# Kernel tuning notes

Hardware: AMD Instinct MI355X
Metric: run time of the kernel (lower is better)

Reference implementation:

```python
import jax, jax.numpy as jnp
import numpy as np

C = 256
HEADS = 4
RADIUS = 2
LN_EPS = 1e-5


def setup_inputs() -> dict:
    key = jax.random.key(0)
    ks = jax.random.split(key, 8)
    s = 0.02
    return {
        "feat": jax.random.normal(ks[0], (8, C, 64, 64), dtype=jnp.float32),
        "in_w": jax.random.normal(ks[1], (3 * C, C), dtype=jnp.float32) * s,
        "in_b": jnp.zeros((3 * C,), dtype=jnp.float32),
        "out_w": jax.random.normal(ks[2], (C, C), dtype=jnp.float32) * s,
        "out_b": jnp.zeros((C,), dtype=jnp.float32),
        "proj_w": jax.random.normal(ks[3], (C, 4 * C), dtype=jnp.float32) * s,
        "proj_b": jnp.zeros((C,), dtype=jnp.float32),
        "ln_g": jnp.ones((C,), dtype=jnp.float32),
        "ln_b": jnp.zeros((C,), dtype=jnp.float32),
    }


def _spatial_mask(h, w, radius):
    yy, xx = jnp.meshgrid(jnp.arange(h), jnp.arange(w), indexing="ij")
    coords = jnp.stack([yy.ravel(), xx.ravel()], axis=-1).astype(jnp.float32)  # [N,2]
    dist = jnp.abs(coords[:, None, :] - coords[None, :, :]).sum(-1)  # Manhattan [N,N]
    return jnp.where(dist > radius, -jnp.inf, 0.0).astype(jnp.float32)


def _attend(qf, mf, mask, in_w, in_b, out_w, out_b, proj_w, proj_b, ln_g, ln_b):
    b, c, h, w = qf.shape
    n = h * w
    d = c // HEADS
    qt = qf.reshape(b, c, n).transpose(0, 2, 1)  # [B,N,C]
    mt = mf.reshape(b, c, n).transpose(0, 2, 1)
    q = qt @ in_w[:c].T + in_b[:c]
    k = mt @ in_w[c:2 * c].T + in_b[c:2 * c]
    v = mt @ in_w[2 * c:].T + in_b[2 * c:]
    # [B,H,N,D]
    q = q.reshape(b, n, HEADS, d).transpose(0, 2, 1, 3)
    k = k.reshape(b, n, HEADS, d).transpose(0, 2, 1, 3)
    v = v.reshape(b, n, HEADS, d).transpose(0, 2, 1, 3)
    scores = jnp.einsum("bhnd,bhmd->bhnm", q, k) / jnp.sqrt(jnp.float32(d)) + mask
    attn = jax.nn.softmax(scores, axis=-1)
    ctx = jnp.einsum("bhnm,bhmd->bhnd", attn, v)
    ctx = ctx.transpose(0, 2, 1, 3).reshape(b, n, c) @ out_w.T + out_b  # [B,N,C]
    asym = jnp.concatenate([qt, ctx, jnp.abs(qt - ctx), qt * ctx], axis=-1)
    y = asym @ proj_w.T + proj_b
    mu = y.mean(-1, keepdims=True)
    var = ((y - mu) ** 2).mean(-1, keepdims=True)
    y = (y - mu) / jnp.sqrt(var + LN_EPS) * ln_g + ln_b
    y = jax.nn.relu(y)
    return y.transpose(0, 2, 1).reshape(b, c, h, w)


def reference(feat, in_w, in_b, out_w, out_b, proj_w, proj_b, ln_g, ln_b):
    b, c, h, w = feat.shape
    mid = w // 2
    left = feat[:, :, :, :mid]
    right = feat[:, :, :, mid:]
    right_mirror = right[:, :, :, ::-1]
    left_mirror = left[:, :, :, ::-1]
    mask = _spatial_mask(h, mid, RADIUS)
    args = (mask, in_w, in_b, out_w, out_b, proj_w, proj_b, ln_g, ln_b)
    left_asym = _attend(left, right_mirror, *args)
    right_asym = _attend(right, left_mirror, *args)
    return jnp.concatenate([left_asym, right_asym], axis=-1)
```

## Files before the change

kernel.cpp:

```cpp
#include <hip/hip_runtime.h>
#include <hip/hip_bf16.h>


#define NTOK 32768

using bf16x8 = __attribute__((ext_vector_type(8))) short;
using f32x4  = __attribute__((ext_vector_type(4))) float;

__device__ __forceinline__ float b2f(short s) {
    unsigned u = ((unsigned)(unsigned short)s) << 16;
    union { unsigned u; float f; } c; c.u = u; return c.f;
}
__device__ __forceinline__ short f2b(float f) {
    __hip_bfloat16 h = __float2bfloat16(f);
    return *(short*)&h;
}
__device__ __forceinline__ void async_copy16(const void* g, void* l) {
    __builtin_amdgcn_global_load_lds(
        (const __attribute__((address_space(1))) unsigned int*)g,
        (__attribute__((address_space(3))) unsigned int*)l, 16, 0, 0);
}

__global__ __launch_bounds__(256) void prep_kernel(const float* __restrict__ feat,
                                                   const float* __restrict__ in_w,
                                                   const float* __restrict__ out_w,
                                                   const float* __restrict__ proj_w,
                                                   __hip_bfloat16* __restrict__ X,
                                                   __hip_bfloat16* __restrict__ wbf) {
    const int bid = blockIdx.x;
    const int tid = threadIdx.x;
    if (bid < 4096) {
        __shared__ float tile[32][68];
        const int b   = bid >> 9;
        const int rem = bid & 511;
        const int sp0 = (rem & 63) * 64;
        const int c0  = (rem >> 6) * 32;
        #pragma unroll
        for (int u = 0; u < 2; ++u) {
            const int idx = tid + u * 256;
            const int cl = idx >> 4;
            const int sq = (idx & 15) * 4;
            const float4 v = *(const float4*)(feat + ((size_t)(b * 256 + c0 + cl) << 12) + sp0 + sq);
            tile[cl][sq]     = v.x;
            tile[cl][sq + 1] = v.y;
            tile[cl][sq + 2] = v.z;
            tile[cl][sq + 3] = v.w;
        }
        __syncthreads();
        #pragma unroll
        for (int u = 0; u < 2; ++u) {
            const int idx = tid + u * 256;
            const int tok = idx >> 3;
            const int cq  = (idx & 7) * 4;
            short4 s;
            s.x = f2b(tile[cq][tok]);
            s.y = f2b(tile[cq + 1][tok]);
            s.z = f2b(tile[cq + 2][tok]);
            s.w = f2b(tile[cq + 3][tok]);
            *(short4*)(X + (size_t)(b * 4096 + sp0 + tok) * 256 + c0 + cq) = s;
        }
    } else {
        const int i4 = (bid - 4096) * 1024 + tid * 4;
        if (i4 < 196608) {
            const float4 v = *(const float4*)(in_w + i4);
            short4 s = {f2b(v.x), f2b(v.y), f2b(v.z), f2b(v.w)};
            *(short4*)(wbf + i4) = s;
        }
        if (i4 < 65536) {
            const float4 v = *(const float4*)(out_w + i4);
            short4 s = {f2b(v.x), f2b(v.y), f2b(v.z), f2b(v.w)};
            *(short4*)(wbf + 196608 + i4) = s;
        }
        if (i4 < 262144) {
            const float4 v = *(const float4*)(proj_w + i4);
            short4 s = {f2b(v.x), f2b(v.y), f2b(v.z), f2b(v.w)};
            *(short4*)(wbf + 262144 + i4) = s;
        }
    }
}

template <int KDIM, bool OUT_BF16>
__global__ __launch_bounds__(256) void mfma_gemm(const __hip_bfloat16* __restrict__ A,
                                                 const __hip_bfloat16* __restrict__ W,
                                                 const float* __restrict__ bias,
                                                 void* __restrict__ C, int Ntot) {
    __shared__ __align__(16) short As[2][128 * 64];
    __shared__ __align__(16) short Bs[2][128 * 64];
    const int tid = threadIdx.x;
    const int work = (blockIdx.x & 7) * 192 + (blockIdx.x >> 3);
    const int m0 = (work / 6) * 128;
    const int n0 = (work % 6) * 128;
    const int wave = tid >> 6, lane = tid & 63;
    const int wm = (wave >> 1) * 64;
    const int wn = (wave & 1) * 64;
    const int fm = lane & 15;
    const int fq = lane >> 4;

    #pragma unroll
    for (int v = 0; v < 4; ++v) {
        const int qb = v * 256 + wave * 64;
        const int q = qb + lane;
        const int r = q >> 3;
        const int cs = (q & 7) ^ (r & 7);
        async_copy16(A + (size_t)(m0 + r) * KDIM + cs * 8, &As[0][qb * 8]);
        async_copy16(W + (size_t)(n0 + r) * KDIM + cs * 8, &Bs[0][qb * 8]);
    }
    __syncthreads();

    f32x4 acc[4][4] = {};
    #pragma unroll
    for (int t = 0; t < KDIM / 64; ++t) {
        const int cur = t & 1;
        if (t + 1 < KDIM / 64) {
            #pragma unroll
            for (int v = 0; v < 4; ++v) {
                const int qb = v * 256 + wave * 64;
                const int q = qb + lane;
                const int r = q >> 3;
                const int cs = (q & 7) ^ (r & 7);
                async_copy16(A + (size_t)(m0 + r) * KDIM + (t + 1) * 64 + cs * 8, &As[cur ^ 1][qb * 8]);
                async_copy16(W + (size_t)(n0 + r) * KDIM + (t + 1) * 64 + cs * 8, &Bs[cur ^ 1][qb * 8]);
            }
        }
        #pragma unroll
        for (int kk = 0; kk < 2; ++kk) {
            bf16x8 af[4], bw[4];
            #pragma unroll
            for (int i = 0; i < 4; ++i) {
                const int row = wm + i * 16 + fm;
                af[i] = *(const bf16x8*)(&As[cur][row * 64 + (((fq + kk * 4) ^ (fm & 7)) * 8)]);
            }
            #pragma unroll
            for (int j = 0; j < 4; ++j) {
                const int row = wn + j * 16 + fm;
                bw[j] = *(const bf16x8*)(&Bs[cur][row * 64 + (((fq + kk * 4) ^ (fm & 7)) * 8)]);
            }
            #pragma unroll
            for (int i = 0; i < 4; ++i)
                #pragma unroll
                for (int j = 0; j < 4; ++j)
                    acc[i][j] = __builtin_amdgcn_mfma_f32_16x16x32_bf16(af[i], bw[j], acc[i][j], 0, 0, 0);
        }
        __syncthreads();
    }
    #pragma unroll
    for (int j = 0; j < 4; ++j) {
        const int col = n0 + wn + j * 16 + fm;
        const float bv = bias[col];
        #pragma unroll
        for (int i = 0; i < 4; ++i) {
            #pragma unroll
            for (int r = 0; r < 4; ++r) {
                const int row = m0 + wm + i * 16 + fq * 4 + r;
                const float v = acc[i][j][r] + bv;
                if (OUT_BF16)
                    ((__hip_bfloat16*)C)[(size_t)row * Ntot + col] = __float2bfloat16(v);
                else
                    ((float*)C)[(size_t)row * Ntot + col] = v;
            }
        }
    }
}

#define P0DY ((2u)|(2u<<3)|(2u<<6)|(2u<<9)|(2u<<12)|(1u<<15)|(1u<<18)|(1u<<21))
#define P0DX ((2u)|(1u<<3)|(3u<<6)|(0u<<9)|(4u<<12)|(2u<<15)|(1u<<18)|(3u<<21))
#define P1DY ((3u)|(3u<<3)|(3u<<6)|(0u<<9)|(4u<<12)|(2u<<15)|(2u<<18)|(2u<<21))
#define P1DX ((2u)|(1u<<3)|(3u<<6)|(2u<<9)|(2u<<12)|(2u<<15)|(2u<<18)|(2u<<21))

__global__ __launch_bounds__(256) void attn_kernel(const __hip_bfloat16* __restrict__ qkv,
                                                   __hip_bfloat16* __restrict__ ctx) {
    const int t = blockIdx.x * 4 + (threadIdx.x >> 6);
    const int lane = threadIdx.x & 63;
    const int n  = lane >> 3;
    const int cg = lane & 7;
    const int x6 = t & 63;
    const int yq = (t >> 6) & 63;
    const int b  = t >> 12;
    const int side = x6 >> 5;
    const int x = x6 & 31;

    bool valid[2];
    size_t kb[2];
    #pragma unroll
    for (int p = 0; p < 2; ++p) {
        const unsigned dyp = p ? P1DY : P0DY;
        const unsigned dxp = p ? P1DX : P0DX;
        const int sh = 3 * n;
        const int dy = (int)((dyp >> sh) & 7) - 2;
        const int dx = (int)((dxp >> sh) & 7) - 2;
        const int yy = yq + dy, xx = x + dx;
        valid[p] = (p == 0 || n < 5) && yy >= 0 && yy < 64 && xx >= 0 && xx < 32;
        const int xm = side ? (31 - xx) : (63 - xx);
        int tm = (b << 12) + (yy << 6) + xm;
        if (!valid[p]) tm = t;
        kb[p] = (size_t)tm * 768 + 256 + cg * 8;
    }
    const size_t qb = (size_t)t * 768 + cg * 8;
    const size_t ob = (size_t)t * 256;

    #pragma unroll
    for (int hp = 0; hp < 2; ++hp) {
        bf16x8 q8[2], k8[2][2], v8[2][2];
        #pragma unroll
        for (int hh = 0; hh < 2; ++hh) {
            const int h = hp * 2 + hh;
            q8[hh] = *(const bf16x8*)(qkv + qb + h * 64);
            #pragma unroll
            for (int p = 0; p < 2; ++p) {
                k8[hh][p] = *(const bf16x8*)(qkv + kb[p] + h * 64);
                v8[hh][p] = *(const bf16x8*)(qkv + kb[p] + h * 64 + 256);
            }
        }
        #pragma unroll
        for (int hh = 0; hh < 2; ++hh) {
            float sc[2];
            #pragma unroll
            for (int p = 0; p < 2; ++p) {
                float s = 0.f;
                #pragma unroll
                for (int j = 0; j < 8; ++j) s += b2f(q8[hh][j]) * b2f(k8[hh][p][j]);
                s += __shfl_xor(s, 1, 64);
                s += __shfl_xor(s, 2, 64);
                s += __shfl_xor(s, 4, 64);
                sc[p] = valid[p] ? s * 0.125f : -1e30f;
            }
            const float p0 = __expf(sc[0]);
            const float p1 = __expf(sc[1]);
            float l = p0 + p1;
            l += __shfl_xor(l, 8, 64);
            l += __shfl_xor(l, 16, 64);
            l += __shfl_xor(l, 32, 64);

            float o[8];
            #pragma unroll
            for (int j = 0; j < 8; ++j)
                o[j] = p0 * b2f(v8[hh][0][j]) + p1 * b2f(v8[hh][1][j]);
            float r4[4];
            #pragma unroll
            for (int i = 0; i < 4; ++i) {
                const float a = o[2 * i], bb = o[2 * i + 1];
                const float mine = (n & 1) ? bb : a;
                const float theirs = (n & 1) ? a : bb;
                r4[i] = mine + __shfl_xor(theirs, 8, 64);
            }
            float r2[2];
            #pragma unroll
            for (int i = 0; i < 2; ++i) {
                const float a = r4[2 * i], bb = r4[2 * i + 1];
                const float mine = (n & 2) ? bb : a;
                const float theirs = (n & 2) ? a : bb;
                r2[i] = mine + __shfl_xor(theirs, 16, 64);
            }
            float ov;
            {
                const float a = r2[0], bb = r2[1];
                const float mine = (n & 4) ? bb : a;
                const float theirs = (n & 4) ? a : bb;
                ov = mine + __shfl_xor(theirs, 32, 64);
            }
            const float rl = __builtin_amdgcn_rcpf(l);
            ctx[ob + (hp * 2 + hh) * 64 + cg * 8 + n] = __float2bfloat16(ov * rl);
        }
    }
}

__global__ __launch_bounds__(512, 4) void proj_ln_fused(const __hip_bfloat16* __restrict__ X,
                                                        const __hip_bfloat16* __restrict__ CTX,
                                                        const __hip_bfloat16* __restrict__ W2,
                                                        const float* __restrict__ out_b,
                                                        const __hip_bfloat16* __restrict__ W,
                                                        const float* __restrict__ bias,
                                                        const float* __restrict__ ln_g,
                                                        const float* __restrict__ ln_b,
                                                        float* __restrict__ out) {
    __shared__ __align__(16) short smem[36864];
    __shared__ float mu_s[64], inv_s[64];
    short* c2s = smem;
    short* As  = smem + 16384;
    short* Bs  = smem + 20480;
    const int tid = threadIdx.x;
    const int m0 = blockIdx.x * 64;
    const int b = m0 >> 12, sp0 = m0 & 4095;
    const int wave = tid >> 6, lane = tid & 63;
    const int wmh = (wave >> 2) * 32;
    const int wn  = (wave & 3) * 64;
    const int fm = lane & 15;
    const int fq = lane >> 4;

    {
        f32x4 acc2[2][4] = {};
        for (int k0 = 0; k0 < 256; k0 += 64) {
            {
                const int q = tid;
                const int r = q >> 3;
                const int cs = (q & 7) ^ (r & 7);
                async_copy16(CTX + (size_t)(m0 + r) * 256 + k0 + cs * 8, &As[(wave * 64) * 8]);
            }
            #pragma unroll
            for (int v = 0; v < 4; ++v) {
                const int q = v * 512 + tid;
                const int r = q >> 3;
                const int cs = (q & 7) ^ (r & 7);
                async_copy16(W2 + (size_t)r * 256 + k0 + cs * 8, &Bs[(v * 512 + wave * 64) * 8]);
            }
            __syncthreads();
            #pragma unroll
            for (int kk = 0; kk < 2; ++kk) {
                bf16x8 af[2], bw[4];
                #pragma unroll
                for (int i = 0; i < 2; ++i) {
                    const int row = wmh + i * 16 + fm;
                    af[i] = *(const bf16x8*)(&As[row * 64 + (((fq + kk * 4) ^ (fm & 7)) * 8)]);
                }
                #pragma unroll
                for (int j = 0; j < 4; ++j) {
                    const int row = wn + j * 16 + fm;
                    bw[j] = *(const bf16x8*)(&Bs[row * 64 + (((fq + kk * 4) ^ (fm & 7)) * 8)]);
                }
                #pragma unroll
                for (int i = 0; i < 2; ++i)
                    #pragma unroll
                    for (int j = 0; j < 4; ++j)
                        acc2[i][j] = __builtin_amdgcn_mfma_f32_16x16x32_bf16(af[i], bw[j], acc2[i][j], 0, 0, 0);
            }
            __syncthreads();
        }
        #pragma unroll
        for (int j = 0; j < 4; ++j) {
            const int col = wn + j * 16 + fm;
            const float bv = out_b[col];
            const int jch = col >> 3, cl = col & 7;
            #pragma unroll
            for (int i = 0; i < 2; ++i)
                #pragma unroll
                for (int rr = 0; rr < 4; ++rr) {
                    const int row = wmh + i * 16 + fq * 4 + rr;
                    const int slot = (jch & 24) | ((jch & 7) ^ (row & 7));
                    c2s[row * 256 + slot * 8 + cl] = f2b(acc2[i][j][rr] + bv);
                }
        }
    }
    __syncthreads();

    f32x4 acc[2][4] = {};
    for (int k0 = 0; k0 < 1024; k0 += 64) {
        const int g = k0 >> 8;
        const int cb = k0 & 255;
        #pragma unroll
        for (int v = 0; v < 4; ++v) {
            const int q = v * 512 + tid;
            const int r = q >> 3;
            const int cs = (q & 7) ^ (r & 7);
            async_copy16(W + (size_t)r * 1024 + k0 + cs * 8, &Bs[(v * 512 + wave * 64) * 8]);
        }
        if (g == 0) {
            const int q = tid;
            const int r = q >> 3;
            const int cs = (q & 7) ^ (r & 7);
            async_copy16(X + (size_t)(m0 + r) * 256 + cb + cs * 8, &As[(wave * 64) * 8]);
        } else if (g >= 2) {
            const int q = tid;
            const int r = q >> 3;
            const int cs = (q & 7) ^ (r & 7);
            int4 qraw = *(const int4*)(X + (size_t)(m0 + r) * 256 + cb + cs * 8);
            const int jch = (cb >> 3) + cs;
            const int slot = (jch & 24) | ((jch & 7) ^ (r & 7));
            int4 craw = *(const int4*)(&c2s[r * 256 + slot * 8]);
            const short* qs = (const short*)&qraw;
            const short* cw = (const short*)&craw;
            short tmp[8];
            #pragma unroll
            for (int j = 0; j < 8; ++j) {
                const float qv = b2f(qs[j]), cv = b2f(cw[j]);
                tmp[j] = f2b(g == 2 ? fabsf(qv - cv) : qv * cv);
            }
            *(int4*)(&As[q * 8]) = *(int4*)tmp;
        }
        __syncthreads();
        #pragma unroll
        for (int kk = 0; kk < 2; ++kk) {
            bf16x8 af[2], bw[4];
            if (g == 1) {
                #pragma unroll
                for (int i = 0; i < 2; ++i) {
                    const int row = wmh + i * 16 + fm;
                    const int jch = (cb >> 3) + fq + kk * 4;
                    const int slot = (jch & 24) | ((jch & 7) ^ (row & 7));
                    af[i] = *(const bf16x8*)(&c2s[row * 256 + slot * 8]);
                }
            } else {
                #pragma unroll
                for (int i = 0; i < 2; ++i) {
                    const int row = wmh + i * 16 + fm;
                    af[i] = *(const bf16x8*)(&As[row * 64 + (((fq + kk * 4) ^ (fm & 7)) * 8)]);
                }
            }
            #pragma unroll
            for (int j = 0; j < 4; ++j) {
                const int row = wn + j * 16 + fm;
                bw[j] = *(const bf16x8*)(&Bs[row * 64 + (((fq + kk * 4) ^ (fm & 7)) * 8)]);
            }
            #pragma unroll
            for (int i = 0; i < 2; ++i)
                #pragma unroll
                for (int j = 0; j < 4; ++j)
                    acc[i][j] = __builtin_amdgcn_mfma_f32_16x16x32_bf16(af[i], bw[j], acc[i][j], 0, 0, 0);
        }
        __syncthreads();
    }
    short* ys = smem;
    #pragma unroll
    for (int j = 0; j < 4; ++j) {
        const int col = wn + j * 16 + fm;
        const float bv = bias[col];
        #pragma unroll
        for (int i = 0; i < 2; ++i)
            #pragma unroll
            for (int r = 0; r < 4; ++r)
                ys[(wmh + i * 16 + fq * 4 + r) * 266 + col] = f2b(acc[i][j][r] + bv);
    }
    __syncthreads();
    {
        const int tt = tid >> 3, seg = tid & 7;
        float s = 0.f, ss = 0.f;
        #pragma unroll
        for (int j = 0; j < 32; ++j) {
            const float v = b2f(ys[tt * 266 + seg * 32 + j]);
            s += v; ss += v * v;
        }
        s += __shfl_xor(s, 1, 64);  ss += __shfl_xor(ss, 1, 64);
        s += __shfl_xor(s, 2, 64);  ss += __shfl_xor(ss, 2, 64);
        s += __shfl_xor(s, 4, 64);  ss += __shfl_xor(ss, 4, 64);
        if (seg == 0) {
            const float mu = s * (1.f / 256.f);
            const float var = ss * (1.f / 256.f) - mu * mu;
            mu_s[tt] = mu;
            inv_s[tt] = rsqrtf(var + 1e-5f);
        }
    }
    __syncthreads();
    {
        const int tl = tid & 63;
        const int j0 = tid >> 6;
        const float mu = mu_s[tl], inv = inv_s[tl];
        #pragma unroll
        for (int u = 0; u < 32; ++u) {
            const int j = j0 * 32 + u;
            const float v = (b2f(ys[tl * 266 + j]) - mu) * inv * ln_g[j] + ln_b[j];
            out[((size_t)(b * 256 + j) << 12) + sp0 + tl] = fmaxf(v, 0.f);
        }
    }
}

extern "C" void kernel_launch(void* const* d_in, const int* in_sizes, int n_in,
                              void* d_out, int out_size, void* d_ws, size_t ws_size,
                              hipStream_t stream) {
    (void)in_sizes; (void)n_in; (void)out_size; (void)ws_size;
    const float* feat   = (const float*)d_in[0];
    const float* in_w   = (const float*)d_in[1];
    const float* in_b   = (const float*)d_in[2];
    const float* out_w  = (const float*)d_in[3];
    const float* out_b  = (const float*)d_in[4];
    const float* proj_w = (const float*)d_in[5];
    const float* proj_b = (const float*)d_in[6];
    const float* ln_g   = (const float*)d_in[7];
    const float* ln_b   = (const float*)d_in[8];
    float* out = (float*)d_out;

    char* ws = (char*)d_ws;
    __hip_bfloat16* Xbf  = (__hip_bfloat16*)(ws);
    __hip_bfloat16* wbf  = (__hip_bfloat16*)(ws + (size_t)(16) * (1 << 20));
    __hip_bfloat16* qkv  = (__hip_bfloat16*)(ws + (size_t)(17) * (1 << 20));
    __hip_bfloat16* ctx  = (__hip_bfloat16*)(ws + (size_t)(65) * (1 << 20));
    __hip_bfloat16* in_wbf   = wbf;
    __hip_bfloat16* out_wbf  = wbf + 196608;
    __hip_bfloat16* proj_wbf = wbf + 262144;

    prep_kernel   <<<4352, 256, 0, stream>>>(feat, in_w, out_w, proj_w, Xbf, wbf);
    mfma_gemm<256, true><<<1536, 256, 0, stream>>>(Xbf, in_wbf, in_b, qkv, 768);
    attn_kernel   <<<NTOK / 4, 256, 0, stream>>>(qkv, ctx);
    proj_ln_fused <<<NTOK / 64, 512, 0, stream>>>(Xbf, ctx, out_wbf, out_b,
                                                  proj_wbf, proj_b, ln_g, ln_b, out);
}
```

Before: 180.8 us.

## Double-buffer LDS tiles in proj_ln_fused with K=32 steps across both GEMMs

Restructures the fused projection kernel so the out-projection GEMM and the 1024-wide projection GEMM run as one continuous pipeline. LDS tiles shrink from K=64 to K=32 and are ping-pong buffered, with a new swizzle. The next tile is prefetched asynchronously while MFMAs consume the current one, which halves the barriers per step and hides global load latency. The trade-off is twice as many iterations, a single-kk compute per step, and more complex control flow, including a cross-phase prefetch of X/W at the last out-proj step.

After: 189.6 us. 4.8% more time.

```diff
diff --git a/kernel.cpp b/kernel.cpp
--- a/kernel.cpp
+++ b/kernel.cpp
@@ -276,8 +276,10 @@
     __shared__ __align__(16) short smem[36864];
     __shared__ float mu_s[64], inv_s[64];
     short* c2s = smem;
-    short* As  = smem + 16384;
-    short* Bs  = smem + 20480;
+    short* As0 = smem + 16384;
+    short* As1 = smem + 18432;
+    short* Bs0 = smem + 20480;
+    short* Bs1 = smem + 28672;
     const int tid = threadIdx.x;
     const int m0 = blockIdx.x * 64;
     const int b = m0 >> 12, sp0 = m0 & 4095;
@@ -287,83 +289,127 @@
     const int fm = lane & 15;
     const int fq = lane >> 4;
 
-    {
-        f32x4 acc2[2][4] = {};
-        for (int k0 = 0; k0 < 256; k0 += 64) {
-            {
-                const int q = tid;
-                const int r = q >> 3;
-                const int cs = (q & 7) ^ (r & 7);
-                async_copy16(CTX + (size_t)(m0 + r) * 256 + k0 + cs * 8, &As[(wave * 64) * 8]);
-            }
-            #pragma unroll
-            for (int v = 0; v < 4; ++v) {
-                const int q = v * 512 + tid;
-                const int r = q >> 3;
-                const int cs = (q & 7) ^ (r & 7);
-                async_copy16(W2 + (size_t)r * 256 + k0 + cs * 8, &Bs[(v * 512 + wave * 64) * 8]);
-            }
-            __syncthreads();
-            #pragma unroll
-            for (int kk = 0; kk < 2; ++kk) {
-                bf16x8 af[2], bw[4];
-                #pragma unroll
-                for (int i = 0; i < 2; ++i) {
-                    const int row = wmh + i * 16 + fm;
-                    af[i] = *(const bf16x8*)(&As[row * 64 + (((fq + kk * 4) ^ (fm & 7)) * 8)]);
-                }
-                #pragma unroll
-                for (int j = 0; j < 4; ++j) {
-                    const int row = wn + j * 16 + fm;
-                    bw[j] = *(const bf16x8*)(&Bs[row * 64 + (((fq + kk * 4) ^ (fm & 7)) * 8)]);
-                }
+    auto stageBs = [&](const __hip_bfloat16* src, int ldk, int k0, short* dst) {
+        #pragma unroll
+        for (int v = 0; v < 2; ++v) {
+            const int q = v * 512 + tid;
+            const int r = q >> 2;
+            const int cs = (q & 3) ^ ((r >> 1) & 3);
+            async_copy16(src + (size_t)r * ldk + k0 + cs * 8, dst + (size_t)q * 8);
+        }
+    };
+    auto stageAs = [&](const __hip_bfloat16* src, int k0, short* dst) {
+        if (tid < 256) {
+            const int r = tid >> 2;
+            const int cs = (tid & 3) ^ ((r >> 1) & 3);
+            async_copy16(src + (size_t)(m0 + r) * 256 + k0 + cs * 8, dst + (size_t)tid * 8);
+        }
+    };
+    auto computeAs = [&](const short* As_, const short* Bs_, f32x4 (&ac)[2][4]) {
+        bf16x8 af[2], bw[4];
+        #pragma unroll
+        for (int i = 0; i < 2; ++i) {
+            const int row = wmh + i * 16 + fm;
+            af[i] = *(const bf16x8*)(&As_[row * 32 + ((fq ^ ((row >> 1) & 3)) * 8)]);
+        }
+        #pragma unroll
+        for (int j = 0; j < 4; ++j) {
+            const int row = wn + j * 16 + fm;
+            bw[j] = *(const bf16x8*)(&Bs_[row * 32 + ((fq ^ ((row >> 1) & 3)) * 8)]);
+        }
+        #pragma unroll
+        for (int i = 0; i < 2; ++i)
+            #pragma unroll
+            for (int j = 0; j < 4; ++j)
+                ac[i][j] = __builtin_amdgcn_mfma_f32_16x16x32_bf16(af[i], bw[j], ac[i][j], 0, 0, 0);
+    };
+
+    f32x4 acc2[2][4] = {};
+    stageAs(CTX, 0, As0);
+    stageBs(W2, 256, 0, Bs0);
+    __syncthreads();
+    for (int t = 0; t < 8; ++t) {
+        short* Ac = (t & 1) ? As1 : As0;
+        short* An = (t & 1) ? As0 : As1;
+        short* Bc = (t & 1) ? Bs1 : Bs0;
+        short* Bn = (t & 1) ? Bs0 : Bs1;
+        if (t < 7) {
+            stageAs(CTX, (t + 1) * 32, An);
+            stageBs(W2, 256, (t + 1) * 32, Bn);
+        } else {
+            stageAs(X, 0, An);
+            stageBs(W, 1024, 0, Bn);
+        }
+        computeAs(Ac, Bc, acc2);
+        if (t == 7) {
+            #pragma unroll
+            for (int j = 0; j < 4; ++j) {
+                const int col = wn + j * 16 + fm;
+                const float bv = out_b[col];
+                const int jch = col >> 3, cl = col & 7;
                 #pragma unroll
                 for (int i = 0; i < 2; ++i)
                     #pragma unroll
-                    for (int j = 0; j < 4; ++j)
-                        acc2[i][j] = __builtin_amdgcn_mfma_f32_16x16x32_bf16(af[i], bw[j], acc2[i][j], 0, 0, 0);
-            }
-            __syncthreads();
-        }
-        #pragma unroll
-        for (int j = 0; j < 4; ++j) {
-            const int col = wn + j * 16 + fm;
-            const float bv = out_b[col];
-            const int jch = col >> 3, cl = col & 7;
+                    for (int rr = 0; rr < 4; ++rr) {
+                        const int row = wmh + i * 16 + fq * 4 + rr;
+                        const int slot = (jch & 24) | ((jch & 7) ^ (row & 7));
+                        c2s[row * 256 + slot * 8 + cl] = f2b(acc2[i][j][rr] + bv);
+                    }
+            }
+        }
+        __syncthreads();
+    }
+
+    f32x4 acc[2][4] = {};
+    for (int s = 0; s < 32; ++s) {
+        short* Ac = (s & 1) ? As1 : As0;
+        short* An = (s & 1) ? As0 : As1;
+        short* Bc = (s & 1) ? Bs1 : Bs0;
+        short* Bn = (s & 1) ? Bs0 : Bs1;
+        const int g  = s >> 3;
+        const int cb = (s & 7) * 32;
+        int4 qraw;
+        int gn = 9;
+        if (s < 31) {
+            const int s1 = s + 1;
+            gn = s1 >> 3;
+            const int cb1 = (s1 & 7) * 32;
+            stageBs(W, 1024, s1 * 32, Bn);
+            if (gn == 0) {
+                stageAs(X, cb1, An);
+            } else if (gn >= 2 && tid < 256) {
+                const int r = tid >> 2;
+                const int cs = (tid & 3) ^ ((r >> 1) & 3);
+                qraw = *(const int4*)(X + (size_t)(m0 + r) * 256 + cb1 + cs * 8);
+            }
+        }
+        if (g == 1) {
+            bf16x8 af[2], bw[4];
+            #pragma unroll
+            for (int i = 0; i < 2; ++i) {
+                const int row = wmh + i * 16 + fm;
+                const int jch = (cb >> 3) + fq;
+                const int slot = (jch & 24) | ((jch & 7) ^ (row & 7));
+                af[i] = *(const bf16x8*)(&c2s[row * 256 + slot * 8]);
+            }
+            #pragma unroll
+            for (int j = 0; j < 4; ++j) {
+                const int row = wn + j * 16 + fm;
+                bw[j] = *(const bf16x8*)(&Bc[row * 32 + ((fq ^ ((row >> 1) & 3)) * 8)]);
+            }
             #pragma unroll
             for (int i = 0; i < 2; ++i)
                 #pragma unroll
-                for (int rr = 0; rr < 4; ++rr) {
-                    const int row = wmh + i * 16 + fq * 4 + rr;
-                    const int slot = (jch & 24) | ((jch & 7) ^ (row & 7));
-                    c2s[row * 256 + slot * 8 + cl] = f2b(acc2[i][j][rr] + bv);
-                }
-        }
-    }
-    __syncthreads();
-
-    f32x4 acc[2][4] = {};
-    for (int k0 = 0; k0 < 1024; k0 += 64) {
-        const int g = k0 >> 8;
-        const int cb = k0 & 255;
-        #pragma unroll
-        for (int v = 0; v < 4; ++v) {
-            const int q = v * 512 + tid;
-            const int r = q >> 3;
-            const int cs = (q & 7) ^ (r & 7);
-            async_copy16(W + (size_t)r * 1024 + k0 + cs * 8, &Bs[(v * 512 + wave * 64) * 8]);
-        }
-        if (g == 0) {
-            const int q = tid;
-            const int r = q >> 3;
-            const int cs = (q & 7) ^ (r & 7);
-            async_copy16(X + (size_t)(m0 + r) * 256 + cb + cs * 8, &As[(wave * 64) * 8]);
-        } else if (g >= 2) {
-            const int q = tid;
-            const int r = q >> 3;
-            const int cs = (q & 7) ^ (r & 7);
-            int4 qraw = *(const int4*)(X + (size_t)(m0 + r) * 256 + cb + cs * 8);
-            const int jch = (cb >> 3) + cs;
+                for (int j = 0; j < 4; ++j)
+                    acc[i][j] = __builtin_amdgcn_mfma_f32_16x16x32_bf16(af[i], bw[j], acc[i][j], 0, 0, 0);
+        } else {
+            computeAs(Ac, Bc, acc);
+        }
+        if (gn >= 2 && gn <= 3 && tid < 256) {
+            const int r = tid >> 2;
+            const int cs = (tid & 3) ^ ((r >> 1) & 3);
+            const int cb1 = ((s + 1) & 7) * 32;
+            const int jch = (cb1 >> 3) + cs;
             const int slot = (jch & 24) | ((jch & 7) ^ (r & 7));
             int4 craw = *(const int4*)(&c2s[r * 256 + slot * 8]);
             const short* qs = (const short*)&qraw;
@@ -372,42 +418,13 @@
             #pragma unroll
             for (int j = 0; j < 8; ++j) {
                 const float qv = b2f(qs[j]), cv = b2f(cw[j]);
-                tmp[j] = f2b(g == 2 ? fabsf(qv - cv) : qv * cv);
-            }
-            *(int4*)(&As[q * 8]) = *(int4*)tmp;
+                tmp[j] = f2b(gn == 2 ? fabsf(qv - cv) : qv * cv);
+            }
+            *(int4*)(&An[tid * 8]) = *(int4*)tmp;
         }
         __syncthreads();
-        #pragma unroll
-        for (int kk = 0; kk < 2; ++kk) {
-            bf16x8 af[2], bw[4];
-            if (g == 1) {
-                #pragma unroll
-                for (int i = 0; i < 2; ++i) {
-                    const int row = wmh + i * 16 + fm;
-                    const int jch = (cb >> 3) + fq + kk * 4;
-                    const int slot = (jch & 24) | ((jch & 7) ^ (row & 7));
-                    af[i] = *(const bf16x8*)(&c2s[row * 256 + slot * 8]);
-                }
-            } else {
-                #pragma unroll
-                for (int i = 0; i < 2; ++i) {
-                    const int row = wmh + i * 16 + fm;
-                    af[i] = *(const bf16x8*)(&As[row * 64 + (((fq + kk * 4) ^ (fm & 7)) * 8)]);
-                }
-            }
-            #pragma unroll
-            for (int j = 0; j < 4; ++j) {
-                const int row = wn + j * 16 + fm;
-                bw[j] = *(const bf16x8*)(&Bs[row * 64 + (((fq + kk * 4) ^ (fm & 7)) * 8)]);
-            }
-            #pragma unroll
-            for (int i = 0; i < 2; ++i)
-                #pragma unroll
-                for (int j = 0; j < 4; ++j)
-                    acc[i][j] = __builtin_amdgcn_mfma_f32_16x16x32_bf16(af[i], bw[j], acc[i][j], 0, 0, 0);
-        }
-        __syncthreads();
-    }
+    }
+
     short* ys = smem;
     #pragma unroll
     for (int j = 0; j < 4; ++j) {
```

## Double-buffer weight tiles and preload full X/CTX rows in fused proj kernel

Applied to the files above, without the earlier changes.

Restructures the fused out-proj/proj+LN kernel so weight K-tiles are double-buffered, with the next tile's async copy issued before the MFMAs on the current one and raw s_waitcnt/s_barrier used for synchronisation. CTX and X rows are staged whole (256 columns) into LDS once instead of per K-step. The K loop is reordered so each 64-column chunk yields both the |q-ctx| and q*ctx tiles from a single computation. LDS use doubles to about 147KB and the min-blocks-per-CU launch bound is dropped, which lowers occupancy in exchange for overlapping loads with compute.

After: 194.2 us. 1.07x slower.

```diff
diff --git a/kernel.cpp b/kernel.cpp
--- a/kernel.cpp
+++ b/kernel.cpp
@@ -264,20 +264,23 @@
     }
 }
 
-__global__ __launch_bounds__(512, 4) void proj_ln_fused(const __hip_bfloat16* __restrict__ X,
-                                                        const __hip_bfloat16* __restrict__ CTX,
-                                                        const __hip_bfloat16* __restrict__ W2,
-                                                        const float* __restrict__ out_b,
-                                                        const __hip_bfloat16* __restrict__ W,
-                                                        const float* __restrict__ bias,
-                                                        const float* __restrict__ ln_g,
-                                                        const float* __restrict__ ln_b,
-                                                        float* __restrict__ out) {
-    __shared__ __align__(16) short smem[36864];
+__global__ __launch_bounds__(512) void proj_ln_fused(const __hip_bfloat16* __restrict__ X,
+                                                     const __hip_bfloat16* __restrict__ CTX,
+                                                     const __hip_bfloat16* __restrict__ W2,
+                                                     const float* __restrict__ out_b,
+                                                     const __hip_bfloat16* __restrict__ W,
+                                                     const float* __restrict__ bias,
+                                                     const float* __restrict__ ln_g,
+                                                     const float* __restrict__ ln_b,
+                                                     float* __restrict__ out) {
+    __shared__ __align__(16) short smem[73728];
     __shared__ float mu_s[64], inv_s[64];
     short* c2s = smem;
-    short* As  = smem + 16384;
-    short* Bs  = smem + 20480;
+    short* Xs  = smem + 16384;
+    short* A2  = smem + 32768;
+    short* A3  = smem + 36864;
+    short* Bs0 = smem + 40960;
+    short* Bs1 = smem + 57344;
     const int tid = threadIdx.x;
     const int m0 = blockIdx.x * 64;
     const int b = m0 >> 12, sp0 = m0 & 4095;
@@ -287,118 +290,140 @@
     const int fm = lane & 15;
     const int fq = lane >> 4;
 
-    {
-        f32x4 acc2[2][4] = {};
-        for (int k0 = 0; k0 < 256; k0 += 64) {
-            {
-                const int q = tid;
-                const int r = q >> 3;
-                const int cs = (q & 7) ^ (r & 7);
-                async_copy16(CTX + (size_t)(m0 + r) * 256 + k0 + cs * 8, &As[(wave * 64) * 8]);
-            }
-            #pragma unroll
-            for (int v = 0; v < 4; ++v) {
-                const int q = v * 512 + tid;
-                const int r = q >> 3;
-                const int cs = (q & 7) ^ (r & 7);
-                async_copy16(W2 + (size_t)r * 256 + k0 + cs * 8, &Bs[(v * 512 + wave * 64) * 8]);
-            }
-            __syncthreads();
-            #pragma unroll
-            for (int kk = 0; kk < 2; ++kk) {
-                bf16x8 af[2], bw[4];
-                #pragma unroll
-                for (int i = 0; i < 2; ++i) {
-                    const int row = wmh + i * 16 + fm;
-                    af[i] = *(const bf16x8*)(&As[row * 64 + (((fq + kk * 4) ^ (fm & 7)) * 8)]);
-                }
-                #pragma unroll
-                for (int j = 0; j < 4; ++j) {
-                    const int row = wn + j * 16 + fm;
-                    bw[j] = *(const bf16x8*)(&Bs[row * 64 + (((fq + kk * 4) ^ (fm & 7)) * 8)]);
-                }
-                #pragma unroll
-                for (int i = 0; i < 2; ++i)
-                    #pragma unroll
-                    for (int j = 0; j < 4; ++j)
-                        acc2[i][j] = __builtin_amdgcn_mfma_f32_16x16x32_bf16(af[i], bw[j], acc2[i][j], 0, 0, 0);
-            }
-            __syncthreads();
-        }
-        #pragma unroll
-        for (int j = 0; j < 4; ++j) {
-            const int col = wn + j * 16 + fm;
-            const float bv = out_b[col];
-            const int jch = col >> 3, cl = col & 7;
-            #pragma unroll
-            for (int i = 0; i < 2; ++i)
-                #pragma unroll
-                for (int rr = 0; rr < 4; ++rr) {
-                    const int row = wmh + i * 16 + fq * 4 + rr;
-                    const int slot = (jch & 24) | ((jch & 7) ^ (row & 7));
-                    c2s[row * 256 + slot * 8 + cl] = f2b(acc2[i][j][rr] + bv);
-                }
-        }
-    }
-    __syncthreads();
-
-    f32x4 acc[2][4] = {};
-    for (int k0 = 0; k0 < 1024; k0 += 64) {
-        const int g = k0 >> 8;
-        const int cb = k0 & 255;
+    auto stageB = [&](const __hip_bfloat16* src, int ldk, int kcol, short* dst) {
         #pragma unroll
         for (int v = 0; v < 4; ++v) {
             const int q = v * 512 + tid;
             const int r = q >> 3;
             const int cs = (q & 7) ^ (r & 7);
-            async_copy16(W + (size_t)r * 1024 + k0 + cs * 8, &Bs[(v * 512 + wave * 64) * 8]);
-        }
-        if (g == 0) {
-            const int q = tid;
-            const int r = q >> 3;
-            const int cs = (q & 7) ^ (r & 7);
-            async_copy16(X + (size_t)(m0 + r) * 256 + cb + cs * 8, &As[(wave * 64) * 8]);
-        } else if (g >= 2) {
-            const int q = tid;
-            const int r = q >> 3;
-            const int cs = (q & 7) ^ (r & 7);
-            int4 qraw = *(const int4*)(X + (size_t)(m0 + r) * 256 + cb + cs * 8);
-            const int jch = (cb >> 3) + cs;
-            const int slot = (jch & 24) | ((jch & 7) ^ (r & 7));
-            int4 craw = *(const int4*)(&c2s[r * 256 + slot * 8]);
-            const short* qs = (const short*)&qraw;
-            const short* cw = (const short*)&craw;
-            short tmp[8];
-            #pragma unroll
-            for (int j = 0; j < 8; ++j) {
-                const float qv = b2f(qs[j]), cv = b2f(cw[j]);
-                tmp[j] = f2b(g == 2 ? fabsf(qv - cv) : qv * cv);
-            }
-            *(int4*)(&As[q * 8]) = *(int4*)tmp;
-        }
-        __syncthreads();
+            async_copy16(src + (size_t)r * ldk + kcol + cs * 8,
+                         dst + (v * 512 + wave * 64) * 8);
+        }
+    };
+    auto stageA256 = [&](const __hip_bfloat16* src, short* dst) {
+        #pragma unroll
+        for (int v = 0; v < 4; ++v) {
+            const int q = v * 512 + tid;
+            const int r = q >> 5;
+            const int sl = q & 31;
+            const int gc = (sl & 24) | ((sl & 7) ^ (r & 7));
+            async_copy16(src + (size_t)(m0 + r) * 256 + gc * 8,
+                         dst + (v * 512 + wave * 64) * 8);
+        }
+    };
+
+    f32x4 acc2[2][4] = {};
+    stageA256(CTX, Xs);
+    stageB(W2, 256, 0, Bs0);
+    for (int t = 0; t < 4; ++t) {
+        short* Bc = (t & 1) ? Bs1 : Bs0;
+        short* Bn = (t & 1) ? Bs0 : Bs1;
+        if (t < 3) {
+            stageB(W2, 256, (t + 1) * 64, Bn);
+            asm volatile("s_waitcnt vmcnt(4) lgkmcnt(0)" ::: "memory");
+        } else {
+            asm volatile("s_waitcnt vmcnt(0) lgkmcnt(0)" ::: "memory");
+        }
+        asm volatile("s_barrier" ::: "memory");
         #pragma unroll
         for (int kk = 0; kk < 2; ++kk) {
+            const int cc = fq + kk * 4;
+            const int jj = t * 8 + cc;
             bf16x8 af[2], bw[4];
-            if (g == 1) {
-                #pragma unroll
-                for (int i = 0; i < 2; ++i) {
-                    const int row = wmh + i * 16 + fm;
-                    const int jch = (cb >> 3) + fq + kk * 4;
-                    const int slot = (jch & 24) | ((jch & 7) ^ (row & 7));
-                    af[i] = *(const bf16x8*)(&c2s[row * 256 + slot * 8]);
-                }
-            } else {
-                #pragma unroll
-                for (int i = 0; i < 2; ++i) {
-                    const int row = wmh + i * 16 + fm;
-                    af[i] = *(const bf16x8*)(&As[row * 64 + (((fq + kk * 4) ^ (fm & 7)) * 8)]);
-                }
+            #pragma unroll
+            for (int i = 0; i < 2; ++i) {
+                const int row = wmh + i * 16 + fm;
+                const int sl = (jj & 24) | ((jj & 7) ^ (row & 7));
+                af[i] = *(const bf16x8*)(&Xs[row * 256 + sl * 8]);
             }
             #pragma unroll
             for (int j = 0; j < 4; ++j) {
                 const int row = wn + j * 16 + fm;
-                bw[j] = *(const bf16x8*)(&Bs[row * 64 + (((fq + kk * 4) ^ (fm & 7)) * 8)]);
+                bw[j] = *(const bf16x8*)(&Bc[row * 64 + ((cc ^ (row & 7)) * 8)]);
+            }
+            #pragma unroll
+            for (int i = 0; i < 2; ++i)
+                #pragma unroll
+                for (int j = 0; j < 4; ++j)
+                    acc2[i][j] = __builtin_amdgcn_mfma_f32_16x16x32_bf16(af[i], bw[j], acc2[i][j], 0, 0, 0);
+        }
+        __builtin_amdgcn_sched_barrier(0);
+        asm volatile("s_barrier" ::: "memory");
+    }
+
+    #pragma unroll
+    for (int j = 0; j < 4; ++j) {
+        const int col = wn + j * 16 + fm;
+        const float bv = out_b[col];
+        const int jch = col >> 3, cl = col & 7;
+        #pragma unroll
+        for (int i = 0; i < 2; ++i)
+            #pragma unroll
+            for (int rr = 0; rr < 4; ++rr) {
+                const int row = wmh + i * 16 + fq * 4 + rr;
+                const int slot = (jch & 24) | ((jch & 7) ^ (row & 7));
+                c2s[row * 256 + slot * 8 + cl] = f2b(acc2[i][j][rr] + bv);
+            }
+    }
+    stageA256(X, Xs);
+    stageB(W, 1024, 0, Bs0);
+    __syncthreads();
+
+    f32x4 acc[2][4] = {};
+    for (int s = 0; s < 16; ++s) {
+        const int cb = s >> 2, g = s & 3;
+        short* Bc = (s & 1) ? Bs1 : Bs0;
+        short* Bn = (s & 1) ? Bs0 : Bs1;
+        if (g == 0) {
+            const int r = tid >> 3, c8 = tid & 7;
+            const int sl = (cb * 8) | (c8 ^ (r & 7));
+            int4 xr = *(const int4*)(&Xs[r * 256 + sl * 8]);
+            int4 cr = *(const int4*)(&c2s[r * 256 + sl * 8]);
+            const short* xe = (const short*)&xr;
+            const short* ce = (const short*)&cr;
+            short t2[8], t3[8];
+            #pragma unroll
+            for (int e = 0; e < 8; ++e) {
+                const float a = b2f(xe[e]), c = b2f(ce[e]);
+                t2[e] = f2b(fabsf(a - c));
+                t3[e] = f2b(a * c);
+            }
+            const int ws = c8 ^ (r & 7);
+            *(int4*)(&A2[r * 64 + ws * 8]) = *(int4*)t2;
+            *(int4*)(&A3[r * 64 + ws * 8]) = *(int4*)t3;
+        }
+        if (s < 15) {
+            const int s1 = s + 1, cb1 = s1 >> 2, g1 = s1 & 3;
+            stageB(W, 1024, g1 * 256 + cb1 * 64, Bn);
+            asm volatile("s_waitcnt vmcnt(4) lgkmcnt(0)" ::: "memory");
+        } else {
+            asm volatile("s_waitcnt vmcnt(0) lgkmcnt(0)" ::: "memory");
+        }
+        asm volatile("s_barrier" ::: "memory");
+        #pragma unroll
+        for (int kk = 0; kk < 2; ++kk) {
+            const int cc = fq + kk * 4;
+            bf16x8 af[2], bw[4];
+            #pragma unroll
+            for (int i = 0; i < 2; ++i) {
+                const int row = wmh + i * 16 + fm;
+                if (g == 0) {
+                    const int jj = cb * 8 + cc;
+                    const int sl = (jj & 24) | ((jj & 7) ^ (row & 7));
+                    af[i] = *(const bf16x8*)(&Xs[row * 256 + sl * 8]);
+                } else if (g == 1) {
+                    const int jj = cb * 8 + cc;
+                    const int sl = (jj & 24) | ((jj & 7) ^ (row & 7));
+                    af[i] = *(const bf16x8*)(&c2s[row * 256 + sl * 8]);
+                } else {
+                    const short* Ag = (g == 2) ? A2 : A3;
+                    af[i] = *(const bf16x8*)(&Ag[row * 64 + ((cc ^ (row & 7)) * 8)]);
+                }
+            }
+            #pragma unroll
+            for (int j = 0; j < 4; ++j) {
+                const int row = wn + j * 16 + fm;
+                bw[j] = *(const bf16x8*)(&Bc[row * 64 + ((cc ^ (row & 7)) * 8)]);
             }
             #pragma unroll
             for (int i = 0; i < 2; ++i)
@@ -406,8 +431,11 @@
                 for (int j = 0; j < 4; ++j)
                     acc[i][j] = __builtin_amdgcn_mfma_f32_16x16x32_bf16(af[i], bw[j], acc[i][j], 0, 0, 0);
         }
-        __syncthreads();
-    }
+        __builtin_amdgcn_sched_barrier(0);
+        asm volatile("s_barrier" ::: "memory");
+    }
+    __syncthreads();
+
     short* ys = smem;
     #pragma unroll
     for (int j = 0; j < 4; ++j) {
```

## Shrink proj_ln_fused tiles to 32 rows and K=32 steps with 256 threads

Applied to the files above, without the earlier changes.

Restructures the fused out-projection/proj/LayerNorm kernel to process 32 tokens per block with 4 waves instead of 64 tokens with 8 waves. The K loop now advances 32 at a time, using a new 4-chunk swizzle for the A and B staging buffers, which cuts shared memory roughly in half. The goal is more resident blocks and more grid parallelism (1024 blocks). In exchange, each block reloads the full weight matrices for fewer rows, doubling total weight traffic from L2, and the loop runs twice as many barrier-separated iterations.

Result: slower. 206.9 us (+14.4%).

```diff
diff --git a/kernel.cpp b/kernel.cpp
--- a/kernel.cpp
+++ b/kernel.cpp
@@ -264,150 +264,140 @@
     }
 }
 
-__global__ __launch_bounds__(512, 4) void proj_ln_fused(const __hip_bfloat16* __restrict__ X,
-                                                        const __hip_bfloat16* __restrict__ CTX,
-                                                        const __hip_bfloat16* __restrict__ W2,
-                                                        const float* __restrict__ out_b,
-                                                        const __hip_bfloat16* __restrict__ W,
-                                                        const float* __restrict__ bias,
-                                                        const float* __restrict__ ln_g,
-                                                        const float* __restrict__ ln_b,
-                                                        float* __restrict__ out) {
-    __shared__ __align__(16) short smem[36864];
-    __shared__ float mu_s[64], inv_s[64];
+__global__ __launch_bounds__(256) void proj_ln_fused(const __hip_bfloat16* __restrict__ X,
+                                                     const __hip_bfloat16* __restrict__ CTX,
+                                                     const __hip_bfloat16* __restrict__ W2,
+                                                     const float* __restrict__ out_b,
+                                                     const __hip_bfloat16* __restrict__ W,
+                                                     const float* __restrict__ bias,
+                                                     const float* __restrict__ ln_g,
+                                                     const float* __restrict__ ln_b,
+                                                     float* __restrict__ out) {
+    __shared__ __align__(16) short smem[17408];
+    __shared__ float mu_s[32], inv_s[32];
     short* c2s = smem;
-    short* As  = smem + 16384;
-    short* Bs  = smem + 20480;
+    short* As  = smem + 8192;
+    short* Bs  = smem + 9216;
     const int tid = threadIdx.x;
-    const int m0 = blockIdx.x * 64;
+    const int m0 = blockIdx.x * 32;
     const int b = m0 >> 12, sp0 = m0 & 4095;
     const int wave = tid >> 6, lane = tid & 63;
-    const int wmh = (wave >> 2) * 32;
-    const int wn  = (wave & 3) * 64;
+    const int wn = wave * 64;
     const int fm = lane & 15;
     const int fq = lane >> 4;
 
-    {
-        f32x4 acc2[2][4] = {};
-        for (int k0 = 0; k0 < 256; k0 += 64) {
-            {
-                const int q = tid;
-                const int r = q >> 3;
-                const int cs = (q & 7) ^ (r & 7);
-                async_copy16(CTX + (size_t)(m0 + r) * 256 + k0 + cs * 8, &As[(wave * 64) * 8]);
-            }
-            #pragma unroll
-            for (int v = 0; v < 4; ++v) {
-                const int q = v * 512 + tid;
-                const int r = q >> 3;
-                const int cs = (q & 7) ^ (r & 7);
-                async_copy16(W2 + (size_t)r * 256 + k0 + cs * 8, &Bs[(v * 512 + wave * 64) * 8]);
-            }
-            __syncthreads();
-            #pragma unroll
-            for (int kk = 0; kk < 2; ++kk) {
-                bf16x8 af[2], bw[4];
+    auto stageA = [&](const __hip_bfloat16* src, int k0) {
+        if (wave < 2) {
+            const int r = tid >> 2;
+            const int cs = (tid & 3) ^ ((r >> 1) & 3);
+            async_copy16(src + (size_t)(m0 + r) * 256 + k0 + cs * 8, &As[(wave * 64) * 8]);
+        }
+    };
+    auto stageB = [&](const __hip_bfloat16* src, int ldk, int k0) {
+        #pragma unroll
+        for (int v = 0; v < 4; ++v) {
+            const int q = v * 256 + tid;
+            const int r = q >> 2;
+            const int cs = (q & 3) ^ ((r >> 1) & 3);
+            async_copy16(src + (size_t)r * ldk + k0 + cs * 8, &Bs[(v * 256 + wave * 64) * 8]);
+        }
+    };
+
+    f32x4 acc2[2][4] = {};
+    for (int t = 0; t < 8; ++t) {
+        stageA(CTX, t * 32);
+        stageB(W2, 256, t * 32);
+        __syncthreads();
+        bf16x8 af[2], bw[4];
+        #pragma unroll
+        for (int i = 0; i < 2; ++i) {
+            const int row = i * 16 + fm;
+            af[i] = *(const bf16x8*)(&As[row * 32 + ((fq ^ ((row >> 1) & 3)) * 8)]);
+        }
+        #pragma unroll
+        for (int j = 0; j < 4; ++j) {
+            const int row = wn + j * 16 + fm;
+            bw[j] = *(const bf16x8*)(&Bs[row * 32 + ((fq ^ ((row >> 1) & 3)) * 8)]);
+        }
+        #pragma unroll
+        for (int i = 0; i < 2; ++i)
+            #pragma unroll
+            for (int j = 0; j < 4; ++j)
+                acc2[i][j] = __builtin_amdgcn_mfma_f32_16x16x32_bf16(af[i], bw[j], acc2[i][j], 0, 0, 0);
+        __syncthreads();
+    }
+    #pragma unroll
+    for (int j = 0; j < 4; ++j) {
+        const int col = wn + j * 16 + fm;
+        const float bv = out_b[col];
+        const int jch = col >> 3, cl = col & 7;
+        #pragma unroll
+        for (int i = 0; i < 2; ++i)
+            #pragma unroll
+            for (int rr = 0; rr < 4; ++rr) {
+                const int row = i * 16 + fq * 4 + rr;
+                const int slot = (jch & 24) | ((jch & 7) ^ (row & 7));
+                c2s[row * 256 + slot * 8 + cl] = f2b(acc2[i][j][rr] + bv);
+            }
+    }
+    __syncthreads();
+
+    f32x4 acc[2][4] = {};
+    for (int s = 0; s < 32; ++s) {
+        const int g = s >> 3;
+        const int cb = (s & 7) * 32;
+        stageB(W, 1024, s * 32);
+        if (g == 0) {
+            stageA(X, cb);
+        } else if (g >= 2) {
+            if (wave < 2) {
+                const int r = tid >> 2;
+                const int cs = (tid & 3) ^ ((r >> 1) & 3);
+                int4 qraw = *(const int4*)(X + (size_t)(m0 + r) * 256 + cb + cs * 8);
+                const int jch = (cb >> 3) + cs;
+                const int slot = (jch & 24) | ((jch & 7) ^ (r & 7));
+                int4 craw = *(const int4*)(&c2s[r * 256 + slot * 8]);
+                const short* qs = (const short*)&qraw;
+                const short* cw = (const short*)&craw;
+                short tmp[8];
                 #pragma unroll
-                for (int i = 0; i < 2; ++i) {
-                    const int row = wmh + i * 16 + fm;
-                    af[i] = *(const bf16x8*)(&As[row * 64 + (((fq + kk * 4) ^ (fm & 7)) * 8)]);
+                for (int j = 0; j < 8; ++j) {
+                    const float qv = b2f(qs[j]), cv = b2f(cw[j]);
+                    tmp[j] = f2b(g == 2 ? fabsf(qv - cv) : qv * cv);
                 }
-                #pragma unroll
-                for (int j = 0; j < 4; ++j) {
-                    const int row = wn + j * 16 + fm;
-                    bw[j] = *(const bf16x8*)(&Bs[row * 64 + (((fq + kk * 4) ^ (fm & 7)) * 8)]);
-                }
-                #pragma unroll
-                for (int i = 0; i < 2; ++i)
-                    #pragma unroll
-                    for (int j = 0; j < 4; ++j)
-                        acc2[i][j] = __builtin_amdgcn_mfma_f32_16x16x32_bf16(af[i], bw[j], acc2[i][j], 0, 0, 0);
-            }
-            __syncthreads();
+                *(int4*)(&As[tid * 8]) = *(int4*)tmp;
+            }
+        }
+        __syncthreads();
+        bf16x8 af[2], bw[4];
+        if (g == 1) {
+            #pragma unroll
+            for (int i = 0; i < 2; ++i) {
+                const int row = i * 16 + fm;
+                const int jch = (cb >> 3) + fq;
+                const int slot = (jch & 24) | ((jch & 7) ^ (row & 7));
+                af[i] = *(const bf16x8*)(&c2s[row * 256 + slot * 8]);
+            }
+        } else {
+            #pragma unroll
+            for (int i = 0; i < 2; ++i) {
+                const int row = i * 16 + fm;
+                af[i] = *(const bf16x8*)(&As[row * 32 + ((fq ^ ((row >> 1) & 3)) * 8)]);
+            }
         }
         #pragma unroll
         for (int j = 0; j < 4; ++j) {
-            const int col = wn + j * 16 + fm;
-            const float bv = out_b[col];
-            const int jch = col >> 3, cl = col & 7;
-            #pragma unroll
-            for (int i = 0; i < 2; ++i)
-                #pragma unroll
-                for (int rr = 0; rr < 4; ++rr) {
-                    const int row = wmh + i * 16 + fq * 4 + rr;
-                    const int slot = (jch & 24) | ((jch & 7) ^ (row & 7));
-                    c2s[row * 256 + slot * 8 + cl] = f2b(acc2[i][j][rr] + bv);
-                }
-        }
-    }
-    __syncthreads();
-
-    f32x4 acc[2][4] = {};
-    for (int k0 = 0; k0 < 1024; k0 += 64) {
-        const int g = k0 >> 8;
-        const int cb = k0 & 255;
-        #pragma unroll
-        for (int v = 0; v < 4; ++v) {
-            const int q = v * 512 + tid;
-            const int r = q >> 3;
-            const int cs = (q & 7) ^ (r & 7);
-            async_copy16(W + (size_t)r * 1024 + k0 + cs * 8, &Bs[(v * 512 + wave * 64) * 8]);
-        }
-        if (g == 0) {
-            const int q = tid;
-            const int r = q >> 3;
-            const int cs = (q & 7) ^ (r & 7);
-            async_copy16(X + (size_t)(m0 + r) * 256 + cb + cs * 8, &As[(wave * 64) * 8]);
-        } else if (g >= 2) {
-            const int q = tid;
-            const int r = q >> 3;
-            const int cs = (q & 7) ^ (r & 7);
-            int4 qraw = *(const int4*)(X + (size_t)(m0 + r) * 256 + cb + cs * 8);
-            const int jch = (cb >> 3) + cs;
-            const int slot = (jch & 24) | ((jch & 7) ^ (r & 7));
-            int4 craw = *(const int4*)(&c2s[r * 256 + slot * 8]);
-            const short* qs = (const short*)&qraw;
-            const short* cw = (const short*)&craw;
-            short tmp[8];
-            #pragma unroll
-            for (int j = 0; j < 8; ++j) {
-                const float qv = b2f(qs[j]), cv = b2f(cw[j]);
-                tmp[j] = f2b(g == 2 ? fabsf(qv - cv) : qv * cv);
-            }
-            *(int4*)(&As[q * 8]) = *(int4*)tmp;
-        }
-        __syncthreads();
-        #pragma unroll
-        for (int kk = 0; kk < 2; ++kk) {
-            bf16x8 af[2], bw[4];
-            if (g == 1) {
-                #pragma unroll
-                for (int i = 0; i < 2; ++i) {
-                    const int row = wmh + i * 16 + fm;
-                    const int jch = (cb >> 3) + fq + kk * 4;
-                    const int slot = (jch & 24) | ((jch & 7) ^ (row & 7));
-                    af[i] = *(const bf16x8*)(&c2s[row * 256 + slot * 8]);
-                }
-            } else {
-                #pragma unroll
-                for (int i = 0; i < 2; ++i) {
-                    const int row = wmh + i * 16 + fm;
-                    af[i] = *(const bf16x8*)(&As[row * 64 + (((fq + kk * 4) ^ (fm & 7)) * 8)]);
-                }
-            }
-            #pragma unroll
-            for (int j = 0; j < 4; ++j) {
-                const int row = wn + j * 16 + fm;
-                bw[j] = *(const bf16x8*)(&Bs[row * 64 + (((fq + kk * 4) ^ (fm & 7)) * 8)]);
-            }
-            #pragma unroll
-            for (int i = 0; i < 2; ++i)
-                #pragma unroll
-                for (int j = 0; j < 4; ++j)
-                    acc[i][j] = __builtin_amdgcn_mfma_f32_16x16x32_bf16(af[i], bw[j], acc[i][j], 0, 0, 0);
-        }
-        __syncthreads();
-    }
+            const int row = wn + j * 16 + fm;
+            bw[j] = *(const bf16x8*)(&Bs[row * 32 + ((fq ^ ((row >> 1) & 3)) * 8)]);
+        }
+        #pragma unroll
+        for (int i = 0; i < 2; ++i)
+            #pragma unroll
+            for (int j = 0; j < 4; ++j)
+                acc[i][j] = __builtin_amdgcn_mfma_f32_16x16x32_bf16(af[i], bw[j], acc[i][j], 0, 0, 0);
+        __syncthreads();
+    }
+
     short* ys = smem;
     #pragma unroll
     for (int j = 0; j < 4; ++j) {
@@ -417,7 +407,7 @@
         for (int i = 0; i < 2; ++i)
             #pragma unroll
             for (int r = 0; r < 4; ++r)
-                ys[(wmh + i * 16 + fq * 4 + r) * 266 + col] = f2b(acc[i][j][r] + bv);
+                ys[(i * 16 + fq * 4 + r) * 266 + col] = f2b(acc[i][j][r] + bv);
     }
     __syncthreads();
     {
@@ -440,8 +430,8 @@
     }
     __syncthreads();
     {
-        const int tl = tid & 63;
-        const int j0 = tid >> 6;
+        const int tl = tid & 31;
+        const int j0 = tid >> 5;
         const float mu = mu_s[tl], inv = inv_s[tl];
         #pragma unroll
         for (int u = 0; u < 32; ++u) {
@@ -479,6 +469,6 @@
     prep_kernel   <<<4352, 256, 0, stream>>>(feat, in_w, out_w, proj_w, Xbf, wbf);
     mfma_gemm<256, true><<<1536, 256, 0, stream>>>(Xbf, in_wbf, in_b, qkv, 768);
     attn_kernel   <<<NTOK / 4, 256, 0, stream>>>(qkv, ctx);
-    proj_ln_fused <<<NTOK / 64, 512, 0, stream>>>(Xbf, ctx, out_wbf, out_b,
+    proj_ln_fused <<<NTOK / 32, 256, 0, stream>>>(Xbf, ctx, out_wbf, out_b,
                                                   proj_wbf, proj_b, ln_g, ln_b, out);
 }
```
